# Optimization experiments

Measured on AMD Instinct MI355X. Metric: run time of the kernel, lower is better.

## Reference

```python
import jax, jax.numpy as jnp
import numpy as np

LOG2 = float(np.log(2.0))
CUTOFF = 10.0
INPUT_DIM = 5


def ssp(x):
    # ShiftedSoftplus
    return jax.nn.softplus(x) - LOG2


def setup_inputs() -> dict:
    key = jax.random.key(0)
    ks = jax.random.split(key, 16)
    N, E, D, G, L = 20000, 320000, 128, 100, 6
    s = 0.05
    return {
        "z": jax.random.normal(ks[0], (N, INPUT_DIM + D), jnp.float32),
        "edge_index": jax.random.randint(ks[1], (2, E), 0, N, dtype=jnp.int64),
        "edge_length": jax.random.uniform(ks[2], (E,), jnp.float32),
        "edge_attr": jax.random.uniform(ks[3], (E, G), jnp.float32),
        "emblin_w": jax.random.normal(ks[4], (D, INPUT_DIM), jnp.float32) * s,
        "emblin_b": jnp.zeros((D,), jnp.float32),
        "mlp_w1": jax.random.normal(ks[5], (L, D, G), jnp.float32) * s,
        "mlp_b1": jnp.zeros((L, D), jnp.float32),
        "mlp_w2": jax.random.normal(ks[6], (L, D, D), jnp.float32) * s,
        "mlp_b2": jnp.zeros((L, D), jnp.float32),
        "lin1_w": jax.random.normal(ks[7], (L, D, D), jnp.float32) * s,
        "lin2_w": jax.random.normal(ks[8], (L, D, D), jnp.float32) * s,
        "lin2_b": jnp.zeros((L, D), jnp.float32),
        "lin_w": jax.random.normal(ks[9], (L, D, 2 * D), jnp.float32) * s,
        "lin_b": jnp.zeros((L, D), jnp.float32),
    }


def reference(z, edge_index, edge_length, edge_attr, emblin_w, emblin_b,
              mlp_w1, mlp_b1, mlp_w2, mlp_b2, lin1_w, lin2_w, lin2_b,
              lin_w, lin_b):
    # time_emb=True path: split z into node features and time embedding
    zf, ptemb = z[:, :INPUT_DIM], z[:, INPUT_DIM:]
    h = zf @ emblin_w.T + emblin_b + ptemb          # [N, D]
    src, dst = edge_index[0], edge_index[1]
    N = h.shape[0]
    # non-smooth cutoff gate: C = (edge_length <= cutoff)
    C = (edge_length <= CUTOFF).astype(h.dtype)     # [E]
    L = mlp_w1.shape[0]
    for l in range(L):
        # edge-wise filter MLP with cutoff gate
        Wf = ssp(edge_attr @ mlp_w1[l].T + mlp_b1[l]) @ mlp_w2[l].T + mlp_b2[l]
        Wf = Wf * C[:, None]                        # [E, F]
        xf = h @ lin1_w[l].T                        # [N, F]
        m_ij = xf[src] * Wf                         # gather + elementwise, [E, F]
        m_i = jax.ops.segment_sum(m_ij, dst, num_segments=N)  # scatter-add, [N, F]
        m = ssp(m_i @ lin2_w[l].T + lin2_b[l])      # [N, D]
        h = h + (jnp.concatenate([h, m], axis=1) @ lin_w[l].T + lin_b[l])
    return h
```

## Files before the change

### kernel.cpp

```cpp
#include <hip/hip_runtime.h>

#define N_NODES 20000
#define D 128
#define E_EDGES 320000
#define G 100
#define L_LAYERS 6
#define IN_DIM 5
#define ZROW (IN_DIM + D)
#define CUTOFF_V 10.0f
#define LOG2F_ 0.69314718055994530942f

typedef __attribute__((ext_vector_type(8))) short bf16x8;
typedef __attribute__((ext_vector_type(4))) float f32x4;
typedef unsigned short ushort_t;
typedef unsigned int uint_t;

__device__ __forceinline__ float sspf(float x) {
    return fmaxf(x, 0.0f) + __logf(1.0f + __expf(-fabsf(x))) - LOG2F_;
}

__device__ __forceinline__ ushort_t f2bf(float f) {
    union { float f; uint_t u; } x; x.f = f;
    uint_t r = ((x.u >> 16) & 1u) + 0x7fffu;
    return (ushort_t)((x.u + r) >> 16);
}

__device__ __forceinline__ uint_t pack2(float a, float b) {
    return (uint_t)f2bf(a) | ((uint_t)f2bf(b) << 16);
}

__device__ __forceinline__ f32x4 mfma_bf16(bf16x8 a, bf16x8 b, f32x4 c) {
    return __builtin_amdgcn_mfma_f32_16x16x32_bf16(a, b, c, 0, 0, 0);
}

__global__ void embed_kernel(const float* __restrict__ z,
                             const float* __restrict__ ew,
                             const float* __restrict__ eb,
                             float* __restrict__ h) {
    int n = blockIdx.x;
    int d = threadIdx.x;
    const float* zr = z + (size_t)n * ZROW;
    float acc = eb[d] + zr[IN_DIM + d];
#pragma unroll
    for (int k = 0; k < IN_DIM; ++k) acc += zr[k] * ew[d * IN_DIM + k];
    h[(size_t)n * D + d] = acc;
}

__global__ void convw1_kernel(const float* __restrict__ w1, ushort_t* __restrict__ out) {
    int idx = blockIdx.x * 256 + threadIdx.x;
    int k = idx & 127;
    int nl = idx >> 7;
    out[idx] = (k < G) ? f2bf(w1[(size_t)nl * G + k]) : (ushort_t)0;
}

__global__ void castbf_kernel(const float* __restrict__ src, ushort_t* __restrict__ dst) {
    int i = blockIdx.x * 256 + threadIdx.x;
    dst[i] = f2bf(src[i]);
}

__global__ void hist_kernel(const int* __restrict__ ei, int* __restrict__ deg) {
    int e = blockIdx.x * 256 + threadIdx.x;
    atomicAdd(&deg[ei[E_EDGES + e]], 1);
}

__global__ __launch_bounds__(1024) void scan_kernel(const int* __restrict__ deg,
                                                    int* __restrict__ row_start,
                                                    int* __restrict__ cursor) {
    __shared__ int wsum[16];
    int t = threadIdx.x;
    const int CH = (N_NODES + 1023) / 1024;
    int base = t * CH;
    int s = 0;
    for (int i = 0; i < CH; ++i) {
        int idx = base + i;
        if (idx < N_NODES) s += deg[idx];
    }
    int lane = t & 63, wid = t >> 6;
    int v = s;
    for (int o = 1; o < 64; o <<= 1) {
        int u = __shfl_up(v, o, 64);
        if (lane >= o) v += u;
    }
    if (lane == 63) wsum[wid] = v;
    __syncthreads();
    if (t == 0) {
        int acc = 0;
        for (int i = 0; i < 16; ++i) { int tmp = wsum[i]; wsum[i] = acc; acc += tmp; }
    }
    __syncthreads();
    int run = v - s + wsum[wid];
    for (int i = 0; i < CH; ++i) {
        int idx = base + i;
        if (idx < N_NODES) {
            row_start[idx] = run;
            cursor[idx] = run;
            run += deg[idx];
        }
    }
    if (t == 0) row_start[N_NODES] = E_EDGES;
}

__global__ void scatter_perm_kernel(const int* __restrict__ ei, const float* __restrict__ el,
                                    int* __restrict__ cursor,
                                    int* __restrict__ perm, int* __restrict__ src_p,
                                    float* __restrict__ cm_p) {
    int e = blockIdx.x * 256 + threadIdx.x;
    int d = ei[E_EDGES + e];
    int p = atomicAdd(&cursor[d], 1);
    perm[p] = e;
    src_p[p] = ei[e];
    cm_p[p] = (el[e] <= CUTOFF_V) ? 1.0f : 0.0f;
}

__global__ void attr_perm_kernel(const float* __restrict__ edge_attr,
                                 const int* __restrict__ perm,
                                 ushort_t* __restrict__ attr_p) {
    int tid = blockIdx.x * 256 + threadIdx.x;
    int r = tid >> 5, ch = tid & 31;
    float4 v = make_float4(0.f, 0.f, 0.f, 0.f);
    if (ch < 25) {
        int pe = perm[r];
        v = *(const float4*)(edge_attr + (size_t)pe * G + ch * 4);
    }
    uint2 p; p.x = pack2(v.x, v.y); p.y = pack2(v.z, v.w);
    *(uint2*)(attr_p + (size_t)r * 128 + ch * 4) = p;
}

__global__ __launch_bounds__(128) void edge_mlp_kernel(
    const ushort_t* __restrict__ attr_p, const float* __restrict__ cm_p,
    const ushort_t* __restrict__ w1b, const float* __restrict__ b1,
    const ushort_t* __restrict__ w2b, const float* __restrict__ b2,
    ushort_t* __restrict__ wf) {
    __shared__ __align__(16) ushort_t sT[32][136];

    int t = threadIdx.x, lane = t & 63, wid = t >> 6;
    int c = lane & 15, quad = lane >> 4;
    int er0 = blockIdx.x * 32;
    int mbase = wid * 64;

    f32x4 acc[2][4];
#pragma unroll
    for (int st = 0; st < 2; ++st)
#pragma unroll
        for (int ct = 0; ct < 4; ++ct) acc[st][ct] = (f32x4){0.f, 0.f, 0.f, 0.f};

#pragma unroll
    for (int ks = 0; ks < 4; ++ks) {
        int koff = ks * 32 + quad * 8;
        bf16x8 b0  = *(const bf16x8*)(attr_p + (size_t)(er0 + c) * 128 + koff);
        bf16x8 b1v = *(const bf16x8*)(attr_p + (size_t)(er0 + 16 + c) * 128 + koff);
#pragma unroll
        for (int ct = 0; ct < 4; ++ct) {
            bf16x8 a = *(const bf16x8*)(w1b + (size_t)(mbase + ct * 16 + c) * 128 + koff);
            acc[0][ct] = mfma_bf16(a, b0, acc[0][ct]);
            acc[1][ct] = mfma_bf16(a, b1v, acc[1][ct]);
        }
    }
#pragma unroll
    for (int st = 0; st < 2; ++st)
#pragma unroll
        for (int ct = 0; ct < 4; ++ct) {
            int col = mbase + ct * 16 + quad * 4;
            float4 bv = *(const float4*)(b1 + col);
            uint2 p;
            p.x = pack2(sspf(acc[st][ct][0] + bv.x), sspf(acc[st][ct][1] + bv.y));
            p.y = pack2(sspf(acc[st][ct][2] + bv.z), sspf(acc[st][ct][3] + bv.w));
            *(uint2*)(&sT[st * 16 + c][col]) = p;
        }

    __syncthreads();

#pragma unroll
    for (int st = 0; st < 2; ++st)
#pragma unroll
        for (int ct = 0; ct < 4; ++ct) acc[st][ct] = (f32x4){0.f, 0.f, 0.f, 0.f};
#pragma unroll
    for (int ks = 0; ks < 4; ++ks) {
        int koff = ks * 32 + quad * 8;
        bf16x8 b0  = *(const bf16x8*)(&sT[c][koff]);
        bf16x8 b1v = *(const bf16x8*)(&sT[16 + c][koff]);
#pragma unroll
        for (int ct = 0; ct < 4; ++ct) {
            bf16x8 a = *(const bf16x8*)(w2b + (size_t)(mbase + ct * 16 + c) * 128 + koff);
            acc[0][ct] = mfma_bf16(a, b0, acc[0][ct]);
            acc[1][ct] = mfma_bf16(a, b1v, acc[1][ct]);
        }
    }
#pragma unroll
    for (int st = 0; st < 2; ++st) {
        int e = er0 + st * 16 + c;
        float cv = cm_p[e];
#pragma unroll
        for (int ct = 0; ct < 4; ++ct) {
            int col = mbase + ct * 16 + quad * 4;
            float4 bv = *(const float4*)(b2 + col);
            uint2 p;
            p.x = pack2((acc[st][ct][0] + bv.x) * cv, (acc[st][ct][1] + bv.y) * cv);
            p.y = pack2((acc[st][ct][2] + bv.z) * cv, (acc[st][ct][3] + bv.w) * cv);
            *(uint2*)(wf + (size_t)e * 128 + col) = p;
        }
    }
}

__global__ __launch_bounds__(256) void lin1_kernel(
    const float* __restrict__ in0, const ushort_t* __restrict__ Wb,
    ushort_t* __restrict__ outp) {
    __shared__ __align__(16) ushort_t sT[32][136];
    int t = threadIdx.x, lane = t & 63, wid = t >> 6;
    int c = lane & 15, quad = lane >> 4;
    int n0 = blockIdx.x * 32;
    int mbase = wid * 32;

    f32x4 acc[2][2];
#pragma unroll
    for (int st = 0; st < 2; ++st)
#pragma unroll
        for (int ct = 0; ct < 2; ++ct) acc[st][ct] = (f32x4){0.f, 0.f, 0.f, 0.f};

#pragma unroll
    for (int i = 0; i < 4; ++i) {
        int idx = i * 256 + t;
        int r = idx >> 5, ch = idx & 31;
        int gr = n0 + r;
        float4 v = make_float4(0.f, 0.f, 0.f, 0.f);
        if (gr < N_NODES) v = *(const float4*)(in0 + (size_t)gr * 128 + ch * 4);
        uint2 p; p.x = pack2(v.x, v.y); p.y = pack2(v.z, v.w);
        *(uint2*)(&sT[r][ch * 4]) = p;
    }
    __syncthreads();
#pragma unroll
    for (int ks = 0; ks < 4; ++ks) {
        int koff = ks * 32 + quad * 8;
        bf16x8 b0  = *(const bf16x8*)(&sT[c][koff]);
        bf16x8 b1v = *(const bf16x8*)(&sT[16 + c][koff]);
#pragma unroll
        for (int ct = 0; ct < 2; ++ct) {
            bf16x8 a = *(const bf16x8*)(Wb + (size_t)(mbase + ct * 16 + c) * 128 + koff);
            acc[0][ct] = mfma_bf16(a, b0, acc[0][ct]);
            acc[1][ct] = mfma_bf16(a, b1v, acc[1][ct]);
        }
    }

#pragma unroll
    for (int st = 0; st < 2; ++st) {
        int node = n0 + st * 16 + c;
        if (node < N_NODES) {
#pragma unroll
            for (int ct = 0; ct < 2; ++ct) {
                int col = mbase + ct * 16 + quad * 4;
                uint2 p;
                p.x = pack2(acc[st][ct][0], acc[st][ct][1]);
                p.y = pack2(acc[st][ct][2], acc[st][ct][3]);
                *(uint2*)(outp + (size_t)node * 128 + col) = p;
            }
        }
    }
}

__global__ __launch_bounds__(256) void fused_tail_kernel(
    const float* __restrict__ m_in, const float* __restrict__ h,
    const ushort_t* __restrict__ W2b, const float* __restrict__ b2,
    const ushort_t* __restrict__ Wub, const float* __restrict__ bu,
    float* __restrict__ h_out) {
    __shared__ __align__(16) ushort_t sT[32][136];
    __shared__ __align__(16) ushort_t sM[32][136];
    int t = threadIdx.x, lane = t & 63, wid = t >> 6;
    int c = lane & 15, quad = lane >> 4;
    int n0 = blockIdx.x * 32;
    int mbase = wid * 32;

    f32x4 acc[2][2];
#pragma unroll
    for (int st = 0; st < 2; ++st)
#pragma unroll
        for (int ct = 0; ct < 2; ++ct) acc[st][ct] = (f32x4){0.f, 0.f, 0.f, 0.f};

#pragma unroll
    for (int i = 0; i < 4; ++i) {
        int idx = i * 256 + t;
        int r = idx >> 5, ch = idx & 31;
        int gr = n0 + r;
        float4 v = make_float4(0.f, 0.f, 0.f, 0.f);
        if (gr < N_NODES) v = *(const float4*)(m_in + (size_t)gr * 128 + ch * 4);
        uint2 p; p.x = pack2(v.x, v.y); p.y = pack2(v.z, v.w);
        *(uint2*)(&sT[r][ch * 4]) = p;
    }
    __syncthreads();
#pragma unroll
    for (int ks = 0; ks < 4; ++ks) {
        int koff = ks * 32 + quad * 8;
        bf16x8 b0  = *(const bf16x8*)(&sT[c][koff]);
        bf16x8 b1v = *(const bf16x8*)(&sT[16 + c][koff]);
#pragma unroll
        for (int ct = 0; ct < 2; ++ct) {
            bf16x8 a = *(const bf16x8*)(W2b + (size_t)(mbase + ct * 16 + c) * 128 + koff);
            acc[0][ct] = mfma_bf16(a, b0, acc[0][ct]);
            acc[1][ct] = mfma_bf16(a, b1v, acc[1][ct]);
        }
    }
#pragma unroll
    for (int st = 0; st < 2; ++st)
#pragma unroll
        for (int ct = 0; ct < 2; ++ct) {
            int col = mbase + ct * 16 + quad * 4;
            float4 bv = *(const float4*)(b2 + col);
            uint2 p;
            p.x = pack2(sspf(acc[st][ct][0] + bv.x), sspf(acc[st][ct][1] + bv.y));
            p.y = pack2(sspf(acc[st][ct][2] + bv.z), sspf(acc[st][ct][3] + bv.w));
            *(uint2*)(&sM[st * 16 + c][col]) = p;
        }
    __syncthreads();

#pragma unroll
    for (int i = 0; i < 4; ++i) {
        int idx = i * 256 + t;
        int r = idx >> 5, ch = idx & 31;
        int gr = n0 + r;
        float4 v = make_float4(0.f, 0.f, 0.f, 0.f);
        if (gr < N_NODES) v = *(const float4*)(h + (size_t)gr * 128 + ch * 4);
        uint2 p; p.x = pack2(v.x, v.y); p.y = pack2(v.z, v.w);
        *(uint2*)(&sT[r][ch * 4]) = p;
    }
    __syncthreads();
#pragma unroll
    for (int st = 0; st < 2; ++st)
#pragma unroll
        for (int ct = 0; ct < 2; ++ct) acc[st][ct] = (f32x4){0.f, 0.f, 0.f, 0.f};
#pragma unroll
    for (int ks = 0; ks < 4; ++ks) {
        int koff = ks * 32 + quad * 8;
        bf16x8 b0  = *(const bf16x8*)(&sT[c][koff]);
        bf16x8 b1v = *(const bf16x8*)(&sT[16 + c][koff]);
#pragma unroll
        for (int ct = 0; ct < 2; ++ct) {
            bf16x8 a = *(const bf16x8*)(Wub + (size_t)(mbase + ct * 16 + c) * 256 + koff);
            acc[0][ct] = mfma_bf16(a, b0, acc[0][ct]);
            acc[1][ct] = mfma_bf16(a, b1v, acc[1][ct]);
        }
    }
#pragma unroll
    for (int ks = 0; ks < 4; ++ks) {
        int koff = ks * 32 + quad * 8;
        bf16x8 b0  = *(const bf16x8*)(&sM[c][koff]);
        bf16x8 b1v = *(const bf16x8*)(&sM[16 + c][koff]);
#pragma unroll
        for (int ct = 0; ct < 2; ++ct) {
            bf16x8 a = *(const bf16x8*)(Wub + (size_t)(mbase + ct * 16 + c) * 256 + 128 + koff);
            acc[0][ct] = mfma_bf16(a, b0, acc[0][ct]);
            acc[1][ct] = mfma_bf16(a, b1v, acc[1][ct]);
        }
    }
#pragma unroll
    for (int st = 0; st < 2; ++st) {
        int node = n0 + st * 16 + c;
        if (node < N_NODES) {
#pragma unroll
            for (int ct = 0; ct < 2; ++ct) {
                int col = mbase + ct * 16 + quad * 4;
                float4 bv = *(const float4*)(bu + col);
                float4 rv = *(const float4*)(h + (size_t)node * 128 + col);
                float4 o;
                o.x = acc[st][ct][0] + bv.x + rv.x;
                o.y = acc[st][ct][1] + bv.y + rv.y;
                o.z = acc[st][ct][2] + bv.z + rv.z;
                o.w = acc[st][ct][3] + bv.w + rv.w;
                *(float4*)(h_out + (size_t)node * 128 + col) = o;
            }
        }
    }
}

__global__ __launch_bounds__(256) void segsum_kernel(
    const ushort_t* __restrict__ wf, const ushort_t* __restrict__ xf_bf,
    const int* __restrict__ row_start, const int* __restrict__ src_p,
    float* __restrict__ m_i) {
    int t = threadIdx.x, lane = t & 63;
    int n = blockIdx.x * 4 + (t >> 6);
    int beg = row_start[n], end = row_start[n + 1];
    float a0 = 0.f, a1 = 0.f;
    for (int i = beg; i < end; ++i) {
        uint_t w = *(const uint_t*)(wf + (size_t)i * 128 + lane * 2);
        uint_t x = *(const uint_t*)(xf_bf + (size_t)src_p[i] * 128 + lane * 2);
        a0 += __uint_as_float(w << 16) * __uint_as_float(x << 16);
        a1 += __uint_as_float(w & 0xffff0000u) * __uint_as_float(x & 0xffff0000u);
    }
    *(float2*)(m_i + (size_t)n * 128 + lane * 2) = make_float2(a0, a1);
}

extern "C" void kernel_launch(void* const* d_in, const int* in_sizes, int n_in,
                              void* d_out, int out_size, void* d_ws, size_t ws_size,
                              hipStream_t stream) {
    const float* z        = (const float*)d_in[0];
    const int*   ei       = (const int*)d_in[1];
    const float* el       = (const float*)d_in[2];
    const float* ea       = (const float*)d_in[3];
    const float* emblin_w = (const float*)d_in[4];
    const float* emblin_b = (const float*)d_in[5];
    const float* mlp_w1   = (const float*)d_in[6];
    const float* mlp_b1   = (const float*)d_in[7];
    const float* mlp_w2   = (const float*)d_in[8];
    const float* mlp_b2   = (const float*)d_in[9];
    const float* lin1_w   = (const float*)d_in[10];
    const float* lin2_w   = (const float*)d_in[11];
    const float* lin2_b   = (const float*)d_in[12];
    const float* lin_w    = (const float*)d_in[13];
    const float* lin_b    = (const float*)d_in[14];
    (void)in_sizes; (void)n_in; (void)out_size; (void)ws_size;

    const size_t ND = (size_t)N_NODES * D;
    float* ws   = (float*)d_ws;
    float* h    = ws;
    float* m_i  = h + ND;
    float* cm_p = m_i + ND;
    float* fend = cm_p + E_EDGES;

    ushort_t* w1b    = (ushort_t*)fend;
    ushort_t* w2b    = w1b   + (size_t)L_LAYERS * D * 128;
    ushort_t* lin1b  = w2b   + (size_t)L_LAYERS * D * D;
    ushort_t* lin2b  = lin1b + (size_t)L_LAYERS * D * D;
    ushort_t* linwb  = lin2b + (size_t)L_LAYERS * D * D;
    ushort_t* wf     = linwb + (size_t)L_LAYERS * D * 256;
    ushort_t* xf_bf  = wf    + (size_t)E_EDGES * 128;
    ushort_t* attr_p = xf_bf + ND;
    int* ibase      = (int*)(attr_p + (size_t)E_EDGES * 128);
    int* deg        = ibase;
    int* row_start  = deg + N_NODES;
    int* cursor     = row_start + N_NODES + 1;
    int* perm       = cursor + N_NODES;
    int* src_p      = perm + E_EDGES;

    convw1_kernel<<<(L_LAYERS * D * 128) / 256, 256, 0, stream>>>(mlp_w1, w1b);
    castbf_kernel<<<(L_LAYERS * D * D) / 256, 256, 0, stream>>>(mlp_w2, w2b);
    castbf_kernel<<<(L_LAYERS * D * D) / 256, 256, 0, stream>>>(lin1_w, lin1b);
    castbf_kernel<<<(L_LAYERS * D * D) / 256, 256, 0, stream>>>(lin2_w, lin2b);
    castbf_kernel<<<(L_LAYERS * D * 256) / 256, 256, 0, stream>>>(lin_w, linwb);

    hipMemsetAsync(deg, 0, (size_t)N_NODES * sizeof(int), stream);
    hist_kernel<<<E_EDGES / 256, 256, 0, stream>>>(ei, deg);
    scan_kernel<<<1, 1024, 0, stream>>>(deg, row_start, cursor);
    scatter_perm_kernel<<<E_EDGES / 256, 256, 0, stream>>>(ei, el, cursor, perm, src_p, cm_p);
    attr_perm_kernel<<<(E_EDGES * 32) / 256, 256, 0, stream>>>(ea, perm, attr_p);

    embed_kernel<<<N_NODES, D, 0, stream>>>(z, emblin_w, emblin_b, h);

    const int NBLK = (N_NODES + 31) / 32;
    for (int l = 0; l < L_LAYERS; ++l) {
        lin1_kernel<<<NBLK, 256, 0, stream>>>(h, lin1b + (size_t)l * D * D, xf_bf);
        edge_mlp_kernel<<<E_EDGES / 32, 128, 0, stream>>>(
            attr_p, cm_p, w1b + (size_t)l * D * 128, mlp_b1 + (size_t)l * D,
            w2b + (size_t)l * D * D, mlp_b2 + (size_t)l * D, wf);
        segsum_kernel<<<N_NODES / 4, 256, 0, stream>>>(wf, xf_bf, row_start, src_p, m_i);
        fused_tail_kernel<<<NBLK, 256, 0, stream>>>(
            m_i, h, lin2b + (size_t)l * D * D, lin2_b + (size_t)l * D,
            linwb + (size_t)l * D * 256, lin_b + (size_t)l * D, h);
    }

    hipMemcpyAsync(d_out, h, ND * sizeof(float), hipMemcpyDeviceToDevice, stream);
}
```

Baseline: 1.401 ms.

## Fuse next-layer lin1 into tail kernel and split segsum edges across half-waves

```diff
diff --git a/kernel.cpp b/kernel.cpp
--- a/kernel.cpp
+++ b/kernel.cpp
@@ -28,6 +28,9 @@
 __device__ __forceinline__ uint_t pack2(float a, float b) {
     return (uint_t)f2bf(a) | ((uint_t)f2bf(b) << 16);
 }
+
+__device__ __forceinline__ float bf16lo(uint_t u) { return __uint_as_float(u << 16); }
+__device__ __forceinline__ float bf16hi(uint_t u) { return __uint_as_float(u & 0xffff0000u); }
 
 __device__ __forceinline__ f32x4 mfma_bf16(bf16x8 a, bf16x8 b, f32x4 c) {
     return __builtin_amdgcn_mfma_f32_16x16x32_bf16(a, b, c, 0, 0, 0);
@@ -257,11 +260,13 @@
     }
 }
 
+template <bool DOLIN1>
 __global__ __launch_bounds__(256) void fused_tail_kernel(
     const float* __restrict__ m_in, const float* __restrict__ h,
     const ushort_t* __restrict__ W2b, const float* __restrict__ b2,
     const ushort_t* __restrict__ Wub, const float* __restrict__ bu,
-    float* __restrict__ h_out) {
+    const ushort_t* __restrict__ lin1n, float* __restrict__ h_out,
+    ushort_t* __restrict__ xf_out) {
     __shared__ __align__(16) ushort_t sT[32][136];
     __shared__ __align__(16) ushort_t sM[32][136];
     int t = threadIdx.x, lane = t & 63, wid = t >> 6;
@@ -350,6 +355,9 @@
             acc[1][ct] = mfma_bf16(a, b1v, acc[1][ct]);
         }
     }
+
+    if (DOLIN1) __syncthreads();
+
 #pragma unroll
     for (int st = 0; st < 2; ++st) {
         int node = n0 + st * 16 + c;
@@ -365,6 +373,44 @@
                 o.z = acc[st][ct][2] + bv.z + rv.z;
                 o.w = acc[st][ct][3] + bv.w + rv.w;
                 *(float4*)(h_out + (size_t)node * 128 + col) = o;
+                if (DOLIN1) {
+                    uint2 p; p.x = pack2(o.x, o.y); p.y = pack2(o.z, o.w);
+                    *(uint2*)(&sT[st * 16 + c][col]) = p;
+                }
+            }
+        }
+    }
+
+    if (DOLIN1) {
+        __syncthreads();
+#pragma unroll
+        for (int st = 0; st < 2; ++st)
+#pragma unroll
+            for (int ct = 0; ct < 2; ++ct) acc[st][ct] = (f32x4){0.f, 0.f, 0.f, 0.f};
+#pragma unroll
+        for (int ks = 0; ks < 4; ++ks) {
+            int koff = ks * 32 + quad * 8;
+            bf16x8 b0  = *(const bf16x8*)(&sT[c][koff]);
+            bf16x8 b1v = *(const bf16x8*)(&sT[16 + c][koff]);
+#pragma unroll
+            for (int ct = 0; ct < 2; ++ct) {
+                bf16x8 a = *(const bf16x8*)(lin1n + (size_t)(mbase + ct * 16 + c) * 128 + koff);
+                acc[0][ct] = mfma_bf16(a, b0, acc[0][ct]);
+                acc[1][ct] = mfma_bf16(a, b1v, acc[1][ct]);
+            }
+        }
+#pragma unroll
+        for (int st = 0; st < 2; ++st) {
+            int node = n0 + st * 16 + c;
+            if (node < N_NODES) {
+#pragma unroll
+                for (int ct = 0; ct < 2; ++ct) {
+                    int col = mbase + ct * 16 + quad * 4;
+                    uint2 p;
+                    p.x = pack2(acc[st][ct][0], acc[st][ct][1]);
+                    p.y = pack2(acc[st][ct][2], acc[st][ct][3]);
+                    *(uint2*)(xf_out + (size_t)node * 128 + col) = p;
+                }
             }
         }
     }
@@ -376,15 +422,24 @@
     float* __restrict__ m_i) {
     int t = threadIdx.x, lane = t & 63;
     int n = blockIdx.x * 4 + (t >> 6);
+    int half = lane >> 5;
+    int cg = (lane & 31) * 4;
     int beg = row_start[n], end = row_start[n + 1];
-    float a0 = 0.f, a1 = 0.f;
-    for (int i = beg; i < end; ++i) {
-        uint_t w = *(const uint_t*)(wf + (size_t)i * 128 + lane * 2);
-        uint_t x = *(const uint_t*)(xf_bf + (size_t)src_p[i] * 128 + lane * 2);
-        a0 += __uint_as_float(w << 16) * __uint_as_float(x << 16);
-        a1 += __uint_as_float(w & 0xffff0000u) * __uint_as_float(x & 0xffff0000u);
-    }
-    *(float2*)(m_i + (size_t)n * 128 + lane * 2) = make_float2(a0, a1);
+    float a0 = 0.f, a1 = 0.f, a2 = 0.f, a3 = 0.f;
+    for (int i = beg + half; i < end; i += 2) {
+        uint2 w = *(const uint2*)(wf + (size_t)i * 128 + cg);
+        uint2 x = *(const uint2*)(xf_bf + (size_t)src_p[i] * 128 + cg);
+        a0 += bf16lo(w.x) * bf16lo(x.x);
+        a1 += bf16hi(w.x) * bf16hi(x.x);
+        a2 += bf16lo(w.y) * bf16lo(x.y);
+        a3 += bf16hi(w.y) * bf16hi(x.y);
+    }
+    a0 += __shfl_xor(a0, 32);
+    a1 += __shfl_xor(a1, 32);
+    a2 += __shfl_xor(a2, 32);
+    a3 += __shfl_xor(a3, 32);
+    if (half == 0)
+        *(float4*)(m_i + (size_t)n * 128 + cg) = make_float4(a0, a1, a2, a3);
 }
 
 extern "C" void kernel_launch(void* const* d_in, const int* in_sizes, int n_in,
@@ -444,15 +499,23 @@
     embed_kernel<<<N_NODES, D, 0, stream>>>(z, emblin_w, emblin_b, h);
 
     const int NBLK = (N_NODES + 31) / 32;
+    lin1_kernel<<<NBLK, 256, 0, stream>>>(h, lin1b, xf_bf);
     for (int l = 0; l < L_LAYERS; ++l) {
-        lin1_kernel<<<NBLK, 256, 0, stream>>>(h, lin1b + (size_t)l * D * D, xf_bf);
         edge_mlp_kernel<<<E_EDGES / 32, 128, 0, stream>>>(
             attr_p, cm_p, w1b + (size_t)l * D * 128, mlp_b1 + (size_t)l * D,
             w2b + (size_t)l * D * D, mlp_b2 + (size_t)l * D, wf);
         segsum_kernel<<<N_NODES / 4, 256, 0, stream>>>(wf, xf_bf, row_start, src_p, m_i);
-        fused_tail_kernel<<<NBLK, 256, 0, stream>>>(
-            m_i, h, lin2b + (size_t)l * D * D, lin2_b + (size_t)l * D,
-            linwb + (size_t)l * D * 256, lin_b + (size_t)l * D, h);
+        if (l + 1 < L_LAYERS) {
+            fused_tail_kernel<true><<<NBLK, 256, 0, stream>>>(
+                m_i, h, lin2b + (size_t)l * D * D, lin2_b + (size_t)l * D,
+                linwb + (size_t)l * D * 256, lin_b + (size_t)l * D,
+                lin1b + (size_t)(l + 1) * D * D, h, xf_bf);
+        } else {
+            fused_tail_kernel<false><<<NBLK, 256, 0, stream>>>(
+                m_i, h, lin2b + (size_t)l * D * D, lin2_b + (size_t)l * D,
+                linwb + (size_t)l * D * 256, lin_b + (size_t)l * D,
+                nullptr, h, nullptr);
+        }
     }
 
     hipMemcpyAsync(d_out, h, ND * sizeof(float), hipMemcpyDeviceToDevice, stream);
```

Result: faster. 1.304 ms (-6.9%).
